# Kernel optimization log

Measured on AMD Instinct MI355X. Metric: run time of the kernel, lower is better.

The kernel has to match this reference:

```python
import jax, jax.numpy as jnp
import numpy as np

D = 256        # d_model
B = 16
T = 8192
K = 100        # num_anchors
EPS = 1e-12    # normalize eps (matches torch sqrt(sum+eps))
LN_EPS = 1e-5  # nn.LayerNorm default
NEG = float(np.finfo(np.float32).min)


def _p(key, shape, scale=0.02):
    return (jax.random.normal(key, shape, dtype=jnp.float32) * scale)


def setup_inputs() -> dict:
    key = jax.random.key(0)
    ks = jax.random.split(key, 12)
    return {
        "vision_tokens": jax.random.normal(ks[0], (B, T, D), dtype=jnp.float32),
        "text_emb": jax.random.normal(ks[1], (B, D), dtype=jnp.float32),
        # fuse: Linear(2D->D), GELU, Linear(D->D)
        "fuse_w1": _p(ks[2], (2 * D, D)), "fuse_b1": jnp.zeros((D,), jnp.float32),
        "fuse_w2": _p(ks[3], (D, D)),     "fuse_b2": jnp.zeros((D,), jnp.float32),
        # box head: LN, Linear(D->D), GELU, Linear(D->4)
        "box_ln_g": jnp.ones((D,), jnp.float32), "box_ln_b": jnp.zeros((D,), jnp.float32),
        "box_w1": _p(ks[4], (D, D)), "box_b1": jnp.zeros((D,), jnp.float32),
        "box_w2": _p(ks[5], (D, 4)), "box_b2": jnp.zeros((4,), jnp.float32),
        # obj head: LN, Linear(D->D), GELU, Linear(D->1)
        "obj_ln_g": jnp.ones((D,), jnp.float32), "obj_ln_b": jnp.zeros((D,), jnp.float32),
        "obj_w1": _p(ks[6], (D, D)), "obj_b1": jnp.zeros((D,), jnp.float32),
        "obj_w2": _p(ks[7], (D, 1)), "obj_b2": jnp.zeros((1,), jnp.float32),
    }


def _layer_norm(x, g, b):
    mu = jnp.mean(x, axis=-1, keepdims=True)
    var = jnp.mean(jnp.square(x - mu), axis=-1, keepdims=True)
    return (x - mu) * jax.lax.rsqrt(var + LN_EPS) * g + b


def _gelu(x):
    return jax.nn.gelu(x, approximate=False)  # torch nn.GELU default is exact erf


def reference(vision_tokens, text_emb,
              fuse_w1, fuse_b1, fuse_w2, fuse_b2,
              box_ln_g, box_ln_b, box_w1, box_b1, box_w2, box_b2,
              obj_ln_g, obj_ln_b, obj_w1, obj_b1, obj_w2, obj_b2):
    # L2-normalize text embedding (sqrt(sum+eps) variant)
    txt = text_emb / jnp.sqrt(jnp.sum(text_emb * text_emb, axis=-1, keepdims=True) + EPS)  # (B,D)
    # broadcast-concat text to every token and fuse
    txt_b = jnp.broadcast_to(txt[:, None, :], vision_tokens.shape)  # (B,T,D)
    cat = jnp.concatenate([vision_tokens, txt_b], axis=-1)          # (B,T,2D)
    h = _gelu(cat @ fuse_w1 + fuse_b1) @ fuse_w2 + fuse_b2          # (B,T,D)
    # box head -> sigmoid xywh
    bh = _layer_norm(h, box_ln_g, box_ln_b)
    boxes = jax.nn.sigmoid(_gelu(bh @ box_w1 + box_b1) @ box_w2 + box_b2)  # (B,T,4)
    # objectness head -> sigmoid score per token
    oh = _layer_norm(h, obj_ln_g, obj_ln_b)
    obj = jax.nn.sigmoid(_gelu(oh @ obj_w1 + obj_b1) @ obj_w2 + obj_b2)[..., 0]  # (B,T)
    # pad with -inf-like min so topk always has K candidates, then clamp idx to T-1
    pad = jnp.full((obj.shape[0], K), NEG, dtype=obj.dtype)
    obj_pad = jnp.concatenate([obj, pad], axis=1)                   # (B,T+K)
    scores, idx_raw = jax.lax.top_k(obj_pad, K)                     # (B,K)
    idx = jnp.minimum(idx_raw, obj.shape[1] - 1)                    # (B,K)
    top_boxes = jnp.take_along_axis(boxes, idx[..., None], axis=1)  # (B,K,4)
    # cosine similarity of fused tokens vs. text
    tok_n = h / jnp.sqrt(jnp.sum(h * h, axis=-1, keepdims=True) + EPS)
    text_scores_full = jnp.sum(tok_n * txt[:, None, :], axis=-1)    # (B,T)
    top_text_scores = jnp.take_along_axis(text_scores_full, idx, axis=1)  # (B,K)
    return (top_boxes, scores, top_text_scores)
```

## Files before the change

### kernel.cpp

```cpp
#include <hip/hip_runtime.h>
#include <math.h>

#define D 256
#define PD 260
#define TOK_B 16
#define TOK_T 8192
#define NTOK (TOK_B * TOK_T)
#define KSEL 100

__device__ float g_txt[TOK_B * D];
__device__ float g_obj[NTOK];
__device__ int   g_sel[TOK_B * KSEL];

template <typename F>
__device__ __forceinline__ float np_sum128_f(F f, int base) {
#pragma clang fp contract(off)
  float r0 = f(base + 0), r1 = f(base + 1), r2 = f(base + 2), r3 = f(base + 3);
  float r4 = f(base + 4), r5 = f(base + 5), r6 = f(base + 6), r7 = f(base + 7);
  for (int i = 8; i < 128; i += 8) {
    r0 += f(base + i + 0); r1 += f(base + i + 1);
    r2 += f(base + i + 2); r3 += f(base + i + 3);
    r4 += f(base + i + 4); r5 += f(base + i + 5);
    r6 += f(base + i + 6); r7 += f(base + i + 7);
  }
  return ((r0 + r1) + (r2 + r3)) + ((r4 + r5) + (r6 + r7));
}
template <typename F>
__device__ __forceinline__ float np_sum256_f(F f) {
#pragma clang fp contract(off)
  return np_sum128_f(f, 0) + np_sum128_f(f, 128);
}

template <typename F>
__device__ __forceinline__ float np_sum256_par8(F f, int j) {
#pragma clang fp contract(off)
  float s0 = f(j);
  for (int i = 1; i < 16; ++i) s0 += f(8 * i + j);
  float s1 = f(128 + j);
  for (int i = 1; i < 16; ++i) s1 += f(128 + 8 * i + j);
  s0 += __shfl_xor(s0, 1);
  s0 += __shfl_xor(s0, 2);
  s0 += __shfl_xor(s0, 4);
  s1 += __shfl_xor(s1, 1);
  s1 += __shfl_xor(s1, 2);
  s1 += __shfl_xor(s1, 4);
  return s0 + s1;
}

__device__ __forceinline__ float np_geluf(float x) {
#pragma clang fp contract(off)
  const float t = x / 1.41421356237309504880f;
  const float e = (float)erf((double)t);
  return (0.5f * x) * (1.0f + e);
}
__device__ __forceinline__ float np_sigmoidf(float x) {
#pragma clang fp contract(off)
  return 1.0f / (1.0f + expf(-x));
}

__global__ __launch_bounds__(256) void k0_txt(const float* __restrict__ text_emb) {
#pragma clang fp contract(off)
  const int b = blockIdx.x, tid = threadIdx.x;
  __shared__ float sSq[D];
  __shared__ float sTot;
  const float e = text_emb[b * D + tid];
  sSq[tid] = e * e;
  __syncthreads();
  if (tid == 0) {
    const float* p = sSq;
    sTot = np_sum256_f([&](int i) { return p[i]; });
  }
  __syncthreads();
  g_txt[b * D + tid] = e / sqrtf(sTot + 1e-12f);
}

__device__ __forceinline__ void gemm_acc(const float (*__restrict__ S)[PD],
                                         const float* __restrict__ W, int r0,
                                         int c0, float acc[4][8]) {
  for (int k = 0; k < D; k += 4) {
    float4 A0 = *(const float4*)&S[r0 + 0][k];
    float4 A1 = *(const float4*)&S[r0 + 1][k];
    float4 A2 = *(const float4*)&S[r0 + 2][k];
    float4 A3 = *(const float4*)&S[r0 + 3][k];
    const float ar[4][4] = {{A0.x, A0.y, A0.z, A0.w},
                            {A1.x, A1.y, A1.z, A1.w},
                            {A2.x, A2.y, A2.z, A2.w},
                            {A3.x, A3.y, A3.z, A3.w}};
#pragma unroll
    for (int kk = 0; kk < 4; ++kk) {
      const float* wr = W + (size_t)(k + kk) * D + c0;
      float4 W0 = *(const float4*)wr;
      float4 W1 = *(const float4*)(wr + 4);
      const float wv[8] = {W0.x, W0.y, W0.z, W0.w, W1.x, W1.y, W1.z, W1.w};
#pragma unroll
      for (int i = 0; i < 4; ++i)
#pragma unroll
        for (int j = 0; j < 8; ++j)
          acc[i][j] = fmaf(ar[i][kk], wv[j], acc[i][j]);
    }
  }
}

__global__ __launch_bounds__(256) void k1_obj(
    const float* __restrict__ vision, const float* __restrict__ fuse_w1,
    const float* __restrict__ fuse_b1, const float* __restrict__ fuse_w2,
    const float* __restrict__ fuse_b2, const float* __restrict__ obj_ln_g,
    const float* __restrict__ obj_ln_b, const float* __restrict__ obj_w1,
    const float* __restrict__ obj_b1, const float* __restrict__ obj_w2,
    const float* __restrict__ obj_b2) {
#pragma clang fp contract(off)
  const int tid = threadIdx.x;
  const int tr = tid >> 5, tc = tid & 31;
  const int r0 = tr << 2, c0 = tc << 3;
  const int blk = blockIdx.x;
  const int batch = blk >> 8;

  __shared__ float sA[32][PD];
  __shared__ float sB[32][PD];
  __shared__ float sTxt[D];
  __shared__ float sMu[32], sRstd[32];

  {
    const float* src = vision + (size_t)blk * (32 * D);
#pragma unroll
    for (int i = 0; i < 8; ++i) {
      const int e = i * 1024 + tid * 4;
      const int row = e >> 8, col = e & 255;
      *(float4*)&sA[row][col] = *(const float4*)(src + e);
    }
    sTxt[tid] = g_txt[batch * D + tid];
  }
  __syncthreads();

  float acc[4][8];
#pragma unroll
  for (int i = 0; i < 4; ++i)
#pragma unroll
    for (int j = 0; j < 8; ++j) acc[i][j] = 0.0f;

  gemm_acc(sA, fuse_w1, r0, c0, acc);
  for (int k = 0; k < D; ++k) {
    const float tv = sTxt[k];
    const float* wr = fuse_w1 + (size_t)(D + k) * D + c0;
    float4 W0 = *(const float4*)wr;
    float4 W1 = *(const float4*)(wr + 4);
    const float wv[8] = {W0.x, W0.y, W0.z, W0.w, W1.x, W1.y, W1.z, W1.w};
#pragma unroll
    for (int i = 0; i < 4; ++i)
#pragma unroll
      for (int j = 0; j < 8; ++j) acc[i][j] = fmaf(tv, wv[j], acc[i][j]);
  }
  {
#pragma unroll
    for (int j2 = 0; j2 < 8; ++j2) {
      const float b = fuse_b1[c0 + j2];
#pragma unroll
      for (int i = 0; i < 4; ++i)
        sB[r0 + i][c0 + j2] = np_geluf(acc[i][j2] + b);
    }
  }
  __syncthreads();

#pragma unroll
  for (int i = 0; i < 4; ++i)
#pragma unroll
    for (int j = 0; j < 8; ++j) acc[i][j] = 0.0f;
  gemm_acc(sB, fuse_w2, r0, c0, acc);
  {
#pragma unroll
    for (int j2 = 0; j2 < 8; ++j2) {
      const float b = fuse_b2[c0 + j2];
#pragma unroll
      for (int i = 0; i < 4; ++i) sA[r0 + i][c0 + j2] = acc[i][j2] + b;
    }
  }
  __syncthreads();

  {
    const int r = tid >> 3, j = tid & 7;
    const float* hrow = &sA[r][0];
    const float mu =
        np_sum256_par8([&](int i) { return hrow[i]; }, j) / 256.0f;
    const float var = np_sum256_par8(
                          [&](int i) {
                            const float d = hrow[i] - mu;
                            return d * d;
                          },
                          j) /
                      256.0f;
    if (j == 0) {
      sMu[r] = mu;
      sRstd[r] = 1.0f / sqrtf(var + 1e-5f);
    }
  }
  __syncthreads();

  {
    const float lg = obj_ln_g[tid], lb = obj_ln_b[tid];
    for (int r = 0; r < 32; ++r) {
      const float t = (sA[r][tid] - sMu[r]) * sRstd[r];
      sB[r][tid] = t * lg + lb;
    }
  }
  __syncthreads();

#pragma unroll
  for (int i = 0; i < 4; ++i)
#pragma unroll
    for (int j = 0; j < 8; ++j) acc[i][j] = 0.0f;
  gemm_acc(sB, obj_w1, r0, c0, acc);
  {
#pragma unroll
    for (int j2 = 0; j2 < 8; ++j2) {
      const float b = obj_b1[c0 + j2];
#pragma unroll
      for (int i = 0; i < 4; ++i)
        sA[r0 + i][c0 + j2] = np_geluf(acc[i][j2] + b);
    }
  }
  __syncthreads();

  if ((tid & 7) == 0) {
    const int row = tid >> 3;
    const float* q = &sA[row][0];
    float L = 0.0f;
    for (int k = 0; k < D; ++k) L = fmaf(q[k], obj_w2[k], L);
    L = L + obj_b2[0];
    g_obj[(size_t)blk * 32 + row] = np_sigmoidf(L);
  }
}

__global__ __launch_bounds__(256) void k2_topk(float* __restrict__ out_scores) {
  const int b = blockIdx.x, tid = threadIdx.x;
  __shared__ unsigned long long sKey[TOK_T];
  __shared__ unsigned long long sRed[4];
  for (int i = tid; i < TOK_T; i += 256) {
    const float s = g_obj[b * TOK_T + i];
    sKey[i] = ((unsigned long long)__float_as_uint(s) << 32) |
              (unsigned)(TOK_T - 1 - i);
  }
  __syncthreads();
  for (int rank = 0; rank < KSEL; ++rank) {
    unsigned long long m = 0ull;
    for (int i = tid; i < TOK_T; i += 256) {
      const unsigned long long v = sKey[i];
      m = v > m ? v : m;
    }
#pragma unroll
    for (int off = 32; off > 0; off >>= 1) {
      const unsigned long long o = __shfl_down(m, off, 64);
      m = o > m ? o : m;
    }
    if ((tid & 63) == 0) sRed[tid >> 6] = m;
    __syncthreads();
    if (tid == 0) {
      unsigned long long w = sRed[0];
#pragma unroll
      for (int i = 1; i < 4; ++i) w = sRed[i] > w ? sRed[i] : w;
      const int idx = (TOK_T - 1) - (int)(unsigned)(w & 0xFFFFFFFFull);
      out_scores[b * KSEL + rank] = __uint_as_float((unsigned)(w >> 32));
      g_sel[b * KSEL + rank] = idx;
      sKey[idx] = 0ull;
    }
    __syncthreads();
  }
}

__global__ __launch_bounds__(256) void k3_box(
    const float* __restrict__ vision, const float* __restrict__ fuse_w1,
    const float* __restrict__ fuse_b1, const float* __restrict__ fuse_w2,
    const float* __restrict__ fuse_b2, const float* __restrict__ box_ln_g,
    const float* __restrict__ box_ln_b, const float* __restrict__ box_w1,
    const float* __restrict__ box_b1, const float* __restrict__ box_w2,
    const float* __restrict__ box_b2, float* __restrict__ out) {
#pragma clang fp contract(off)
  const int tid = threadIdx.x, c = tid;
  __shared__ float sV[8][PD];
  __shared__ float sG[8][PD];
  __shared__ float sH[8][PD];
  __shared__ float sTx[8][PD];
  __shared__ float sMu[8], sRstd[8];
  __shared__ int sIdx[8], sBat[8];
  if (tid < 8) {
    const int e = blockIdx.x * 8 + tid;
    sBat[tid] = e / KSEL;
    sIdx[tid] = g_sel[e];
  }
  __syncthreads();
  {
    const int u = tid >> 5, col = (tid & 31) * 8;
    const float* src = vision + ((size_t)sBat[u] * TOK_T + sIdx[u]) * D + col;
    *(float4*)&sV[u][col] = *(const float4*)src;
    *(float4*)&sV[u][col + 4] = *(const float4*)(src + 4);
    const float* tsrc = &g_txt[sBat[u] * D + col];
    *(float4*)&sTx[u][col] = *(const float4*)tsrc;
    *(float4*)&sTx[u][col + 4] = *(const float4*)(tsrc + 4);
  }
  __syncthreads();

  float acc[8];
#pragma unroll
  for (int u = 0; u < 8; ++u) acc[u] = 0.0f;
  for (int k = 0; k < D; ++k) {
    const float w = fuse_w1[k * D + c];
#pragma unroll
    for (int u = 0; u < 8; ++u) acc[u] = fmaf(sV[u][k], w, acc[u]);
  }
  for (int k = 0; k < D; ++k) {
    const float w = fuse_w1[(D + k) * D + c];
#pragma unroll
    for (int u = 0; u < 8; ++u) acc[u] = fmaf(sTx[u][k], w, acc[u]);
  }
  {
    const float b = fuse_b1[c];
#pragma unroll
    for (int u = 0; u < 8; ++u) sG[u][c] = np_geluf(acc[u] + b);
  }
  __syncthreads();

#pragma unroll
  for (int u = 0; u < 8; ++u) acc[u] = 0.0f;
  for (int k = 0; k < D; ++k) {
    const float w = fuse_w2[k * D + c];
#pragma unroll
    for (int u = 0; u < 8; ++u) acc[u] = fmaf(sG[u][k], w, acc[u]);
  }
  {
    const float b = fuse_b2[c];
#pragma unroll
    for (int u = 0; u < 8; ++u) sH[u][c] = acc[u] + b;
  }
  __syncthreads();

  if (tid < 8) {
    const int u = tid;
    const float* h = &sH[u][0];
    const float* tx = &sTx[u][0];
    const float mu = np_sum256_f([&](int i) { return h[i]; }) / 256.0f;
    const float var = np_sum256_f([&](int i) {
                        const float d = h[i] - mu;
                        return d * d;
                      }) / 256.0f;
    sMu[u] = mu;
    sRstd[u] = 1.0f / sqrtf(var + 1e-5f);
    const float q2 = np_sum256_f([&](int i) { return h[i] * h[i]; });
    const float den = sqrtf(q2 + 1e-12f);
    const float ts = np_sum256_f([&](int i) { return (h[i] / den) * tx[i]; });
    out[8000 + blockIdx.x * 8 + u] = ts;
  }
  __syncthreads();

  {
    const float lg = box_ln_g[c], lb = box_ln_b[c];
#pragma unroll
    for (int u = 0; u < 8; ++u) {
      const float t = (sH[u][c] - sMu[u]) * sRstd[u];
      sG[u][c] = t * lg + lb;
    }
  }
  __syncthreads();

#pragma unroll
  for (int u = 0; u < 8; ++u) acc[u] = 0.0f;
  for (int k = 0; k < D; ++k) {
    const float w = box_w1[k * D + c];
#pragma unroll
    for (int u = 0; u < 8; ++u) acc[u] = fmaf(sG[u][k], w, acc[u]);
  }
  {
    const float b = box_b1[c];
#pragma unroll
    for (int u = 0; u < 8; ++u) sV[u][c] = np_geluf(acc[u] + b);
  }
  __syncthreads();

  if (tid < 32) {
    const int u = tid >> 2, j = tid & 3;
    const float* q = &sV[u][0];
    float L = 0.0f;
    for (int k = 0; k < D; ++k) L = fmaf(q[k], box_w2[k * 4 + j], L);
    L = L + box_b2[j];
    out[(blockIdx.x * 8 + u) * 4 + j] = np_sigmoidf(L);
  }
}

extern "C" void kernel_launch(void* const* d_in, const int* in_sizes, int n_in,
                              void* d_out, int out_size, void* d_ws,
                              size_t ws_size, hipStream_t stream) {
  const float* vision   = (const float*)d_in[0];
  const float* text_emb = (const float*)d_in[1];
  const float* fuse_w1  = (const float*)d_in[2];
  const float* fuse_b1  = (const float*)d_in[3];
  const float* fuse_w2  = (const float*)d_in[4];
  const float* fuse_b2  = (const float*)d_in[5];
  const float* box_ln_g = (const float*)d_in[6];
  const float* box_ln_b = (const float*)d_in[7];
  const float* box_w1   = (const float*)d_in[8];
  const float* box_b1   = (const float*)d_in[9];
  const float* box_w2   = (const float*)d_in[10];
  const float* box_b2   = (const float*)d_in[11];
  const float* obj_ln_g = (const float*)d_in[12];
  const float* obj_ln_b = (const float*)d_in[13];
  const float* obj_w1   = (const float*)d_in[14];
  const float* obj_b1   = (const float*)d_in[15];
  const float* obj_w2   = (const float*)d_in[16];
  const float* obj_b2   = (const float*)d_in[17];
  float* out = (float*)d_out;

  k0_txt<<<TOK_B, 256, 0, stream>>>(text_emb);
  k1_obj<<<NTOK / 32, 256, 0, stream>>>(
      vision, fuse_w1, fuse_b1, fuse_w2, fuse_b2, obj_ln_g, obj_ln_b, obj_w1,
      obj_b1, obj_w2, obj_b2);
  k2_topk<<<TOK_B, 256, 0, stream>>>(out + 6400);
  k3_box<<<(TOK_B * KSEL) / 8, 256, 0, stream>>>(
      vision, fuse_w1, fuse_b1, fuse_w2, fuse_b2, box_ln_g, box_ln_b, box_w1,
      box_b1, box_w2, box_b2, out);
}
```

Before: 1.575 ms.

## Use two-level group-max top-k, halve k1 shared memory, parallelize k3 row reductions

```diff
diff --git a/kernel.cpp b/kernel.cpp
--- a/kernel.cpp
+++ b/kernel.cpp
@@ -7,6 +7,8 @@
 #define TOK_T 8192
 #define NTOK (TOK_B * TOK_T)
 #define KSEL 100
+
+typedef unsigned long long ull;
 
 __device__ float g_txt[TOK_B * D];
 __device__ float g_obj[NTOK];
@@ -116,7 +118,6 @@
   const int batch = blk >> 8;
 
   __shared__ float sA[32][PD];
-  __shared__ float sB[32][PD];
   __shared__ float sTxt[D];
   __shared__ float sMu[32], sRstd[32];
 
@@ -150,13 +151,14 @@
 #pragma unroll
       for (int j = 0; j < 8; ++j) acc[i][j] = fmaf(tv, wv[j], acc[i][j]);
   }
+  __syncthreads();
   {
 #pragma unroll
     for (int j2 = 0; j2 < 8; ++j2) {
       const float b = fuse_b1[c0 + j2];
 #pragma unroll
       for (int i = 0; i < 4; ++i)
-        sB[r0 + i][c0 + j2] = np_geluf(acc[i][j2] + b);
+        sA[r0 + i][c0 + j2] = np_geluf(acc[i][j2] + b);
     }
   }
   __syncthreads();
@@ -165,7 +167,8 @@
   for (int i = 0; i < 4; ++i)
 #pragma unroll
     for (int j = 0; j < 8; ++j) acc[i][j] = 0.0f;
-  gemm_acc(sB, fuse_w2, r0, c0, acc);
+  gemm_acc(sA, fuse_w2, r0, c0, acc);
+  __syncthreads();
   {
 #pragma unroll
     for (int j2 = 0; j2 < 8; ++j2) {
@@ -199,7 +202,7 @@
     const float lg = obj_ln_g[tid], lb = obj_ln_b[tid];
     for (int r = 0; r < 32; ++r) {
       const float t = (sA[r][tid] - sMu[r]) * sRstd[r];
-      sB[r][tid] = t * lg + lb;
+      sA[r][tid] = t * lg + lb;
     }
   }
   __syncthreads();
@@ -208,7 +211,8 @@
   for (int i = 0; i < 4; ++i)
 #pragma unroll
     for (int j = 0; j < 8; ++j) acc[i][j] = 0.0f;
-  gemm_acc(sB, obj_w1, r0, c0, acc);
+  gemm_acc(sA, obj_w1, r0, c0, acc);
+  __syncthreads();
   {
 #pragma unroll
     for (int j2 = 0; j2 < 8; ++j2) {
@@ -232,35 +236,51 @@
 
 __global__ __launch_bounds__(256) void k2_topk(float* __restrict__ out_scores) {
   const int b = blockIdx.x, tid = threadIdx.x;
-  __shared__ unsigned long long sKey[TOK_T];
-  __shared__ unsigned long long sRed[4];
+  __shared__ ull sKey[TOK_T];
+  __shared__ ull sGmax[128];
+  __shared__ int sWin;
   for (int i = tid; i < TOK_T; i += 256) {
     const float s = g_obj[b * TOK_T + i];
-    sKey[i] = ((unsigned long long)__float_as_uint(s) << 32) |
-              (unsigned)(TOK_T - 1 - i);
-  }
-  __syncthreads();
-  for (int rank = 0; rank < KSEL; ++rank) {
-    unsigned long long m = 0ull;
-    for (int i = tid; i < TOK_T; i += 256) {
-      const unsigned long long v = sKey[i];
+    sKey[i] = ((ull)__float_as_uint(s) << 32) | (unsigned)(TOK_T - 1 - i);
+  }
+  __syncthreads();
+  if (tid < 128) {
+    ull m = 0ull;
+    for (int j = 0; j < 64; ++j) {
+      const ull v = sKey[tid + 128 * j];
       m = v > m ? v : m;
     }
-#pragma unroll
-    for (int off = 32; off > 0; off >>= 1) {
-      const unsigned long long o = __shfl_down(m, off, 64);
-      m = o > m ? o : m;
-    }
-    if ((tid & 63) == 0) sRed[tid >> 6] = m;
+    sGmax[tid] = m;
+  }
+  __syncthreads();
+  for (int r = 0; r < KSEL; ++r) {
+    if (tid < 64) {
+      ull m = sGmax[tid];
+      const ull o = sGmax[64 + tid];
+      if (o > m) m = o;
+#pragma unroll
+      for (int off = 32; off > 0; off >>= 1) {
+        const ull o2 = __shfl_down(m, off, 64);
+        if (o2 > m) m = o2;
+      }
+      if (tid == 0) {
+        const int idx = (TOK_T - 1) - (int)(unsigned)(m & 0xFFFFFFFFull);
+        out_scores[b * KSEL + r] = __uint_as_float((unsigned)(m >> 32));
+        g_sel[b * KSEL + r] = idx;
+        sKey[idx] = 0ull;
+        sWin = idx & 127;
+      }
+    }
     __syncthreads();
-    if (tid == 0) {
-      unsigned long long w = sRed[0];
-#pragma unroll
-      for (int i = 1; i < 4; ++i) w = sRed[i] > w ? sRed[i] : w;
-      const int idx = (TOK_T - 1) - (int)(unsigned)(w & 0xFFFFFFFFull);
-      out_scores[b * KSEL + rank] = __uint_as_float((unsigned)(w >> 32));
-      g_sel[b * KSEL + rank] = idx;
-      sKey[idx] = 0ull;
+    if (tid < 64) {
+      const int g = sWin;
+      ull v = sKey[g + 128 * tid];
+#pragma unroll
+      for (int off = 32; off > 0; off >>= 1) {
+        const ull o = __shfl_down(v, off, 64);
+        if (o > v) v = o;
+      }
+      if (tid == 0) sGmax[g] = v;
     }
     __syncthreads();
   }
@@ -332,21 +352,29 @@
   }
   __syncthreads();
 
-  if (tid < 8) {
-    const int u = tid;
-    const float* h = &sH[u][0];
-    const float* tx = &sTx[u][0];
-    const float mu = np_sum256_f([&](int i) { return h[i]; }) / 256.0f;
-    const float var = np_sum256_f([&](int i) {
-                        const float d = h[i] - mu;
-                        return d * d;
-                      }) / 256.0f;
-    sMu[u] = mu;
-    sRstd[u] = 1.0f / sqrtf(var + 1e-5f);
-    const float q2 = np_sum256_f([&](int i) { return h[i] * h[i]; });
-    const float den = sqrtf(q2 + 1e-12f);
-    const float ts = np_sum256_f([&](int i) { return (h[i] / den) * tx[i]; });
-    out[8000 + blockIdx.x * 8 + u] = ts;
+  {
+    const int u = tid >> 3, j = tid & 7;
+    if (u < 8) {
+      const float* h = &sH[u][0];
+      const float* tx = &sTx[u][0];
+      const float mu = np_sum256_par8([&](int i) { return h[i]; }, j) / 256.0f;
+      const float var = np_sum256_par8(
+                            [&](int i) {
+                              const float d = h[i] - mu;
+                              return d * d;
+                            },
+                            j) /
+                        256.0f;
+      const float q2 = np_sum256_par8([&](int i) { return h[i] * h[i]; }, j);
+      const float den = sqrtf(q2 + 1e-12f);
+      const float ts =
+          np_sum256_par8([&](int i) { return (h[i] / den) * tx[i]; }, j);
+      if (j == 0) {
+        sMu[u] = mu;
+        sRstd[u] = 1.0f / sqrtf(var + 1e-5f);
+        out[8000 + blockIdx.x * 8 + u] = ts;
+      }
+    }
   }
   __syncthreads();
 
```

Measured after the change: 1.404 ms. 10.8% less time.
